# Kernel optimization log

Measured on AMD Instinct MI355X. Metric: run time of the kernel, lower is better.

## Reference

```python
import jax, jax.numpy as jnp
import numpy as np
import math

B, S, D, H = 4, 1024, 1024, 16
HD = D // H
R = 128  # max_rel_pos
EPS = 1e-5

def setup_inputs() -> dict:
    key = jax.random.key(0)
    ks = jax.random.split(key, 20)
    sd = 1.0 / math.sqrt(D)
    def lin(k, din, dout):
        return jax.random.normal(k, (din, dout), jnp.float32) * (1.0 / math.sqrt(din))
    return {
        "x": jax.random.normal(ks[0], (B, S, D), jnp.float32),
        "wq": lin(ks[1], D, D), "bq": jnp.zeros((D,), jnp.float32),
        "wk": lin(ks[2], D, D), "bk": jnp.zeros((D,), jnp.float32),
        "wv": lin(ks[3], D, D), "bv": jnp.zeros((D,), jnp.float32),
        "wo": lin(ks[4], D, D), "bo": jnp.zeros((D,), jnp.float32),
        "rel_embed": jax.random.normal(ks[5], (2 * R + 1, HD), jnp.float32),
        "ln1_g": jnp.ones((D,), jnp.float32), "ln1_b": jnp.zeros((D,), jnp.float32),
        "ln2_g": jnp.ones((D,), jnp.float32), "ln2_b": jnp.zeros((D,), jnp.float32),
        "w1": lin(ks[6], D, 4 * D), "b1": jnp.zeros((4 * D,), jnp.float32),
        "w2": lin(ks[7], 4 * D, D), "b2": jnp.zeros((D,), jnp.float32),
    }

def _layernorm(x, g, b):
    mu = jnp.mean(x, axis=-1, keepdims=True)
    var = jnp.mean(jnp.square(x - mu), axis=-1, keepdims=True)
    return (x - mu) * jax.lax.rsqrt(var + EPS) * g + b

def _block(x, wq, bq, wk, bk, wv, bv, wo, bo, rel_embed,
           ln1_g, ln1_b, ln2_g, ln2_b, w1, b1, w2, b2):
    h = _layernorm(x, ln1_g, ln1_b)
    # project and split heads: [B,S,D] -> [B,H,S,HD]
    def heads(y):
        return y.reshape(B, S, H, HD).transpose(0, 2, 1, 3)
    Q = heads(h @ wq + bq)
    K = heads(h @ wk + bk)
    V = heads(h @ wv + bv)
    scale = 1.0 / math.sqrt(HD)
    scores = jnp.einsum("bhqd,bhkd->bhqk", Q, K) * scale
    # relative positions: clamp(q-k, -R, R) + R
    pos = jnp.arange(S)
    rel_idx = jnp.clip(pos[None, :] - pos[:, None], -R, R) + R  # [S,S]
    rel = rel_embed[rel_idx]  # [S,S,HD]
    scores = scores + jnp.einsum("bhqd,qkd->bhqk", Q, rel) * scale
    attn = jax.nn.softmax(scores, axis=-1)
    out = jnp.einsum("bhqk,bhkd->bhqd", attn, V)
    out = out.transpose(0, 2, 1, 3).reshape(B, S, D) @ wo + bo
    x = x + out  # dropout is identity in eval
    h2 = _layernorm(x, ln2_g, ln2_b)
    ff = jax.nn.gelu(h2 @ w1 + b1, approximate=False) @ w2 + b2
    return x + ff

def reference(x, wq, bq, wk, bk, wv, bv, wo, bo, rel_embed,
              ln1_g, ln1_b, ln2_g, ln2_b, w1, b1, w2, b2):
    return _block(x, wq, bq, wk, bk, wv, bv, wo, bo, rel_embed,
                  ln1_g, ln1_b, ln2_g, ln2_b, w1, b1, w2, b2)
```

## Files before the change

kernel.cpp:

```cpp
#include <hip/hip_runtime.h>

typedef unsigned short u16;
typedef __bf16 bf16x8 __attribute__((ext_vector_type(8)));
typedef float f32x4 __attribute__((ext_vector_type(4)));

#define QSCALE 0.18033688011112042f

__device__ __forceinline__ float b2f(u16 x) {
    unsigned int u = ((unsigned int)x) << 16;
    return __builtin_bit_cast(float, u);
}
__device__ __forceinline__ u16 f2bf(float f) {
    unsigned int u = __builtin_bit_cast(unsigned int, f);
    u += 0x7fffu + ((u >> 16) & 1u);
    return (u16)(u >> 16);
}
__device__ __forceinline__ void lds_load16(const u16* g, u16* l) {
    __builtin_amdgcn_global_load_lds(
        (const __attribute__((address_space(1))) void*)g,
        (__attribute__((address_space(3))) void*)l, 16, 0, 0);
}

__global__ void transpose_f32_bf16(const float* __restrict__ in, u16* __restrict__ out,
                                   int R, int C) {
    __shared__ u16 tile[32][33];
    int bx = blockIdx.x * 32, by = blockIdx.y * 32;
    int tx = threadIdx.x, ty = threadIdx.y;
#pragma unroll
    for (int i = 0; i < 32; i += 8)
        tile[ty + i][tx] = f2bf(in[(size_t)(by + ty + i) * C + bx + tx]);
    __syncthreads();
#pragma unroll
    for (int i = 0; i < 32; i += 8)
        out[(size_t)(bx + ty + i) * R + by + tx] = tile[tx][ty + i];
}

__global__ void transpose_w4(const float* __restrict__ wq, const float* __restrict__ wk,
                             const float* __restrict__ wv, const float* __restrict__ wo,
                             u16* __restrict__ wqkvT, u16* __restrict__ woT) {
    __shared__ u16 tile[32][33];
    int z = blockIdx.z;
    const float* in = (z == 0) ? wq : (z == 1) ? wk : (z == 2) ? wv : wo;
    u16* out = (z < 3) ? (wqkvT + (size_t)z * 1024 * 1024) : woT;
    int bx = blockIdx.x * 32, by = blockIdx.y * 32;
    int tx = threadIdx.x, ty = threadIdx.y;
#pragma unroll
    for (int i = 0; i < 32; i += 8)
        tile[ty + i][tx] = f2bf(in[(size_t)(by + ty + i) * 1024 + bx + tx]);
    __syncthreads();
#pragma unroll
    for (int i = 0; i < 32; i += 8)
        out[(size_t)(bx + ty + i) * 1024 + by + tx] = tile[tx][ty + i];
}

__global__ void transpose_v(const u16* __restrict__ in, int ldin, int coloff,
                            u16* __restrict__ out) {
    __shared__ u16 tile[32][33];
    size_t zout = (size_t)blockIdx.z << 20;
    int bx = blockIdx.x * 32, by = blockIdx.y * 32;
    int tx = threadIdx.x, ty = threadIdx.y;
#pragma unroll
    for (int i = 0; i < 32; i += 8)
        tile[ty + i][tx] =
            in[(size_t)(blockIdx.z * 1024 + by + ty + i) * ldin + coloff + bx + tx];
    __syncthreads();
#pragma unroll
    for (int i = 0; i < 32; i += 8)
        out[zout + (size_t)(bx + ty + i) * 1024 + by + tx] = tile[tx][ty + i];
}

__global__ void cvt_f32_bf16(const float* __restrict__ in, u16* __restrict__ out, int n) {
    int i = blockIdx.x * 256 + threadIdx.x;
    if (i < n) out[i] = f2bf(in[i]);
}

__global__ void concat3(const float* a, const float* b, const float* c, float* o) {
    int i = blockIdx.x * 256 + threadIdx.x;
    o[i] = (i < 1024) ? a[i] : (i < 2048 ? b[i - 1024] : c[i - 2048]);
}

__global__ __launch_bounds__(256) void ln_kernel(
    const u16* __restrict__ inb, const float* __restrict__ inf,
    const float* __restrict__ g, const float* __restrict__ b,
    u16* __restrict__ out) {
    int row = blockIdx.x, t = threadIdx.x;
    size_t base = (size_t)row * 1024 + t * 4;
    float v[4];
    if (inf) {
        float4 f = *(const float4*)(inf + base);
        v[0] = f.x; v[1] = f.y; v[2] = f.z; v[3] = f.w;
    } else {
        uint2 u = *(const uint2*)(inb + base);
        v[0] = b2f((u16)(u.x & 0xffff)); v[1] = b2f((u16)(u.x >> 16));
        v[2] = b2f((u16)(u.y & 0xffff)); v[3] = b2f((u16)(u.y >> 16));
    }
    float s = v[0] + v[1] + v[2] + v[3];
    float q = v[0] * v[0] + v[1] * v[1] + v[2] * v[2] + v[3] * v[3];
#pragma unroll
    for (int m = 1; m < 64; m <<= 1) {
        s += __shfl_xor(s, m);
        q += __shfl_xor(q, m);
    }
    __shared__ float rs[4], rq[4];
    __shared__ float mu_s, rstd_s;
    int w = t >> 6, lane = t & 63;
    if (lane == 0) { rs[w] = s; rq[w] = q; }
    __syncthreads();
    if (t == 0) {
        float S = rs[0] + rs[1] + rs[2] + rs[3];
        float Q2 = rq[0] + rq[1] + rq[2] + rq[3];
        float mu = S * (1.0f / 1024.0f);
        float var = Q2 * (1.0f / 1024.0f) - mu * mu;
        mu_s = mu;
        rstd_s = rsqrtf(var + 1e-5f);
    }
    __syncthreads();
    float mu = mu_s, rstd = rstd_s;
    u16 o[4];
#pragma unroll
    for (int i = 0; i < 4; i++) {
        int col = t * 4 + i;
        o[i] = f2bf((v[i] - mu) * rstd * g[col] + b[col]);
    }
    uint2 pk;
    pk.x = (unsigned)o[0] | ((unsigned)o[1] << 16);
    pk.y = (unsigned)o[2] | ((unsigned)o[3] << 16);
    *(uint2*)(out + base) = pk;
}

__global__ __launch_bounds__(256) void gemm_bt64(
    const u16* __restrict__ A, int lda,
    const u16* __restrict__ Bt, int ldb,
    const float* __restrict__ bias,
    const float* __restrict__ resid_f32, const u16* __restrict__ resid_bf,
    u16* __restrict__ outb, float* __restrict__ outf, int ldc,
    int K, float oscale, int gelu) {
    constexpr int AU = 16, BU = 8, UPW = (AU + BU) / 4;
    __shared__ __align__(16) u16 As[2][128 * 64];
    __shared__ __align__(16) u16 Bs[2][64 * 64];
    int t = threadIdx.x, w = t >> 6, lane = t & 63;
    int m0 = blockIdx.y * 128, n0 = blockIdx.x * 64;
    int lo = lane & 15, hi = lane >> 4;
    int wr = w >> 1, wc = w & 1;
    f32x4 acc[4][2];
#pragma unroll
    for (int i = 0; i < 4; i++)
#pragma unroll
        for (int j = 0; j < 2; j++) acc[i][j] = (f32x4){0.f, 0.f, 0.f, 0.f};

    auto stage = [&](int k0, int buf) {
#pragma unroll
        for (int uu = 0; uu < UPW; ++uu) {
            int u = w * UPW + uu;
            if (u < AU) {
                int s = u * 64 + lane;
                int row = s >> 3, cg = (lane & 7) ^ (row & 7);
                lds_load16(A + (size_t)(m0 + row) * lda + k0 + cg * 8,
                           &As[buf][u * 512]);
            } else {
                int u2 = u - AU;
                int s = u2 * 64 + lane;
                int row = s >> 3, cg = (lane & 7) ^ (row & 7);
                lds_load16(Bt + (size_t)(n0 + row) * ldb + k0 + cg * 8,
                           &Bs[buf][u2 * 512]);
            }
        }
    };

    int nk = K >> 6;
    stage(0, 0);
    for (int kk = 0; kk < nk; ++kk) {
        __syncthreads();
        if (kk + 1 < nk) stage((kk + 1) << 6, (kk + 1) & 1);
        int buf = kk & 1;
#pragma unroll
        for (int k2 = 0; k2 < 2; ++k2) {
            bf16x8 a[4], bb[2];
#pragma unroll
            for (int i = 0; i < 4; i++) {
                int row = wr * 64 + i * 16 + lo;
                int g = (k2 * 4 + hi) ^ (row & 7);
                a[i] = *(const bf16x8*)&As[buf][row * 64 + g * 8];
            }
#pragma unroll
            for (int j = 0; j < 2; j++) {
                int row = wc * 32 + j * 16 + lo;
                int g = (k2 * 4 + hi) ^ (row & 7);
                bb[j] = *(const bf16x8*)&Bs[buf][row * 64 + g * 8];
            }
#pragma unroll
            for (int i = 0; i < 4; i++)
#pragma unroll
                for (int j = 0; j < 2; j++)
                    acc[i][j] = __builtin_amdgcn_mfma_f32_16x16x32_bf16(a[i], bb[j], acc[i][j], 0, 0, 0);
        }
    }
#pragma unroll
    for (int j = 0; j < 2; j++) {
        int col = n0 + wc * 32 + j * 16 + lo;
        float bv = bias ? bias[col] : 0.f;
#pragma unroll
        for (int i = 0; i < 4; i++) {
            int rbase = m0 + wr * 64 + i * 16 + hi * 4;
#pragma unroll
            for (int r = 0; r < 4; r++) {
                float v = fmaf(acc[i][j][r], oscale, bv);
                if (gelu) v = 0.5f * v * (1.f + erff(v * 0.70710678118654752f));
                size_t ridx = (size_t)(rbase + r) * ldc + col;
                if (resid_f32) v += resid_f32[ridx];
                if (resid_bf) v += b2f(resid_bf[ridx]);
                if (outf) outf[ridx] = v;
                if (outb) outb[ridx] = f2bf(v);
            }
        }
    }
}

__global__ __launch_bounds__(256) void gemm_bt128k64(
    const u16* __restrict__ A, int lda,
    const u16* __restrict__ Bt, int ldb,
    const float* __restrict__ bias,
    u16* __restrict__ outb, int ldc,
    int K, float oscale, int gelu) {
    __shared__ __align__(16) u16 As[2][128 * 64];
    __shared__ __align__(16) u16 Bs[2][128 * 64];
    int t = threadIdx.x, w = t >> 6, lane = t & 63;
    int m0 = blockIdx.y * 128, n0 = blockIdx.x * 128;
    int lo = lane & 15, hi = lane >> 4;
    int wr = w >> 1, wc = w & 1;
    f32x4 acc[4][4];
#pragma unroll
    for (int i = 0; i < 4; i++)
#pragma unroll
        for (int j = 0; j < 4; j++) acc[i][j] = (f32x4){0.f, 0.f, 0.f, 0.f};

    auto stage = [&](int k0, int buf) {
#pragma unroll
        for (int uu = 0; uu < 4; ++uu) {
            int u = w * 4 + uu;
            int s = u * 64 + lane;
            int row = s >> 3, cg = (lane & 7) ^ (row & 7);
            lds_load16(A + (size_t)(m0 + row) * lda + k0 + cg * 8,
                       &As[buf][u * 512]);
        }
#pragma unroll
        for (int uu = 0; uu < 4; ++uu) {
            int u = w * 4 + uu;
            int s = u * 64 + lane;
            int row = s >> 3, cg = (lane & 7) ^ (row & 7);
            lds_load16(Bt + (size_t)(n0 + row) * ldb + k0 + cg * 8,
                       &Bs[buf][u * 512]);
        }
    };

    int nk = K >> 6;
    stage(0, 0);
    for (int kk = 0; kk < nk; ++kk) {
        __syncthreads();
        if (kk + 1 < nk) stage((kk + 1) << 6, (kk + 1) & 1);
        int buf = kk & 1;
#pragma unroll
        for (int k2 = 0; k2 < 2; ++k2) {
            bf16x8 a[4], bb[4];
#pragma unroll
            for (int i = 0; i < 4; i++) {
                int row = wr * 64 + i * 16 + lo;
                int g = (k2 * 4 + hi) ^ (row & 7);
                a[i] = *(const bf16x8*)&As[buf][row * 64 + g * 8];
            }
#pragma unroll
            for (int j = 0; j < 4; j++) {
                int row = wc * 64 + j * 16 + lo;
                int g = (k2 * 4 + hi) ^ (row & 7);
                bb[j] = *(const bf16x8*)&Bs[buf][row * 64 + g * 8];
            }
#pragma unroll
            for (int i = 0; i < 4; i++)
#pragma unroll
                for (int j = 0; j < 4; j++)
                    acc[i][j] = __builtin_amdgcn_mfma_f32_16x16x32_bf16(a[i], bb[j], acc[i][j], 0, 0, 0);
        }
    }
#pragma unroll
    for (int j = 0; j < 4; j++) {
        int col = n0 + wc * 64 + j * 16 + lo;
        float bv = bias ? bias[col] : 0.f;
#pragma unroll
        for (int i = 0; i < 4; i++) {
            int rbase = m0 + wr * 64 + i * 16 + hi * 4;
#pragma unroll
            for (int r = 0; r < 4; r++) {
                float v = fmaf(acc[i][j][r], oscale, bv);
                if (gelu) v = 0.5f * v * (1.f + erff(v * 0.70710678118654752f));
                outb[(size_t)(rbase + r) * ldc + col] = f2bf(v);
            }
        }
    }
}

__global__ __launch_bounds__(256) void attn_kernel(
    const u16* __restrict__ QKV, const u16* __restrict__ Vtg,
    const u16* __restrict__ relb, u16* __restrict__ Ob) {
    __shared__ __align__(16) u16 KsL[2][4096];
    __shared__ __align__(16) u16 VsL[2][4096];
    __shared__ __align__(16) u16 Ps[4][16 * 72];
    __shared__ __align__(16) u16 Rb[4][16 * 280];
    int t = threadIdx.x, w = t >> 6, lane = t & 63;
    int bid = blockIdx.x;
    int qblk = bid & 15, h = (bid >> 4) & 15, bb = bid >> 8;
    int lo = lane & 15, hi = lane >> 4;
    int q0b = qblk * 64;
    int q0 = q0b + w * 16;

    const u16* qrow = QKV + ((size_t)(bb * 1024 + q0 + lo) * 3072 + h * 64 + hi * 8);
    bf16x8 qf0 = *(const bf16x8*)qrow;
    bf16x8 qf1 = *(const bf16x8*)(qrow + 32);

    const u16* Kg = QKV + 1024 + ((size_t)(bb * 1024)) * 3072 + h * 64;
    const u16* Vg = Vtg + ((size_t)(bb * 1024 + h * 64)) * 1024;

    auto stage = [&](int k0, int buf) {
#pragma unroll
        for (int half = 0; half < 2; ++half) {
            int s = half * 256 + w * 64 + lane;
            int row = s >> 3, cg = (s & 7) ^ (row & 7);
            lds_load16(Kg + (size_t)(k0 + row) * 3072 + cg * 8,
                       &KsL[buf][(half * 256 + w * 64) * 8]);
            lds_load16(Vg + (size_t)row * 1024 + k0 + cg * 8,
                       &VsL[buf][(half * 256 + w * 64) * 8]);
        }
    };

    stage(0, 0);

#pragma unroll 4
    for (int pt = 0; pt < 17; ++pt) {
        bf16x8 rf0 = *(const bf16x8*)&relb[(pt * 16 + lo) * 64 + hi * 8];
        bf16x8 rf1 = *(const bf16x8*)&relb[(pt * 16 + lo) * 64 + 32 + hi * 8];
        f32x4 cz = (f32x4){0.f, 0.f, 0.f, 0.f};
        cz = __builtin_amdgcn_mfma_f32_16x16x32_bf16(qf0, rf0, cz, 0, 0, 0);
        cz = __builtin_amdgcn_mfma_f32_16x16x32_bf16(qf1, rf1, cz, 0, 0, 0);
#pragma unroll
        for (int r = 0; r < 4; r++)
            Rb[w][(hi * 4 + r) * 280 + pt * 16 + lo] =
                f2bf(fmaf(cz[r], QSCALE, -16.0f));
    }
    float blo[4], bhi[4];
#pragma unroll
    for (int r = 0; r < 4; r++) {
        blo[r] = b2f(Rb[w][(hi * 4 + r) * 280]);
        bhi[r] = b2f(Rb[w][(hi * 4 + r) * 280 + 256]);
    }

    f32x4 oacc[4];
#pragma unroll
    for (int j = 0; j < 4; j++) oacc[j] = (f32x4){0.f, 0.f, 0.f, 0.f};
    float l_[4] = {0.f, 0.f, 0.f, 0.f};

    for (int c = 0; c < 16; ++c) {
        int k0 = c * 64;
        __syncthreads();
        if (c < 15) stage(k0 + 64, (c + 1) & 1);
        const u16* Ksb = KsL[c & 1];
        const u16* Vsb = VsL[c & 1];

        f32x4 sc[4];
#pragma unroll
        for (int kt = 0; kt < 4; kt++) {
            int row = kt * 16 + lo, rx = row & 7;
            bf16x8 kf0 = *(const bf16x8*)&Ksb[(row * 8 + (hi ^ rx)) * 8];
            bf16x8 kf1 = *(const bf16x8*)&Ksb[(row * 8 + ((4 + hi) ^ rx)) * 8];
            f32x4 zz = (f32x4){0.f, 0.f, 0.f, 0.f};
            sc[kt] = __builtin_amdgcn_mfma_f32_16x16x32_bf16(qf0, kf0, zz, 0, 0, 0);
            sc[kt] = __builtin_amdgcn_mfma_f32_16x16x32_bf16(qf1, kf1, sc[kt], 0, 0, 0);
        }
        float bt[4][4];
        if (k0 + 192 <= q0b) {
#pragma unroll
            for (int kt = 0; kt < 4; kt++)
#pragma unroll
                for (int r = 0; r < 4; r++) bt[kt][r] = blo[r];
        } else if (k0 >= q0b + 192) {
#pragma unroll
            for (int kt = 0; kt < 4; kt++)
#pragma unroll
                for (int r = 0; r < 4; r++) bt[kt][r] = bhi[r];
        } else {
#pragma unroll
            for (int kt = 0; kt < 4; kt++)
#pragma unroll
                for (int r = 0; r < 4; r++) {
                    int lq = hi * 4 + r;
                    int p = (k0 + kt * 16 + lo) - (q0 + lq);
                    p = p < -128 ? -128 : (p > 128 ? 128 : p);
                    p += 128;
                    bt[kt][r] = b2f(Rb[w][lq * 280 + p]);
                }
        }
#pragma unroll
        for (int kt = 0; kt < 4; kt++)
#pragma unroll
            for (int r = 0; r < 4; r++) {
                float s = fmaf(sc[kt][r], QSCALE, bt[kt][r]);
                float p = __builtin_amdgcn_exp2f(s);
                l_[r] += p;
                Ps[w][(hi * 4 + r) * 72 + kt * 16 + lo] =
                    (u16)(__builtin_bit_cast(unsigned int, p) >> 16);
            }
        bf16x8 pf0 = *(const bf16x8*)&Ps[w][lo * 72 + 8 * hi];
        bf16x8 pf1 = *(const bf16x8*)&Ps[w][lo * 72 + 32 + 8 * hi];
#pragma unroll
        for (int j = 0; j < 4; j++) {
            int row = j * 16 + lo, rx = row & 7;
            bf16x8 vf0 = *(const bf16x8*)&Vsb[(row * 8 + (hi ^ rx)) * 8];
            bf16x8 vf1 = *(const bf16x8*)&Vsb[(row * 8 + ((4 + hi) ^ rx)) * 8];
            oacc[j] = __builtin_amdgcn_mfma_f32_16x16x32_bf16(pf0, vf0, oacc[j], 0, 0, 0);
            oacc[j] = __builtin_amdgcn_mfma_f32_16x16x32_bf16(pf1, vf1, oacc[j], 0, 0, 0);
        }
    }
#pragma unroll
    for (int r = 0; r < 4; r++) {
#pragma unroll
        for (int m = 1; m < 16; m <<= 1) l_[r] += __shfl_xor(l_[r], m);
    }
#pragma unroll
    for (int r = 0; r < 4; r++) {
        float inv = 1.f / l_[r];
        int q = q0 + hi * 4 + r;
#pragma unroll
        for (int j = 0; j < 4; j++)
            Ob[(size_t)(bb * 1024 + q) * 1024 + h * 64 + j * 16 + lo] =
                f2bf(oacc[j][r] * inv);
    }
}

extern "C" void kernel_launch(void* const* d_in, const int* in_sizes, int n_in,
                              void* d_out, int out_size, void* d_ws, size_t ws_size,
                              hipStream_t stream) {
    const float* x   = (const float*)d_in[0];
    const float* wq  = (const float*)d_in[1];
    const float* bq  = (const float*)d_in[2];
    const float* wk  = (const float*)d_in[3];
    const float* bk  = (const float*)d_in[4];
    const float* wv  = (const float*)d_in[5];
    const float* bv  = (const float*)d_in[6];
    const float* wo  = (const float*)d_in[7];
    const float* bo  = (const float*)d_in[8];
    const float* rel = (const float*)d_in[9];
    const float* g1  = (const float*)d_in[10];
    const float* be1 = (const float*)d_in[11];
    const float* g2  = (const float*)d_in[12];
    const float* be2 = (const float*)d_in[13];
    const float* w1  = (const float*)d_in[14];
    const float* bf1 = (const float*)d_in[15];
    const float* w2  = (const float*)d_in[16];
    const float* bf2 = (const float*)d_in[17];

    char* ws = (char*)d_ws;
    const size_t MB = 1024ull * 1024ull;
    u16* wqkvT = (u16*)(ws + 0 * MB);
    u16* woT  = (u16*)(ws + 6 * MB);
    u16* w1T  = (u16*)(ws + 8 * MB);
    u16* w2T  = (u16*)(ws + 16 * MB);
    u16* h    = (u16*)(ws + 24 * MB);
    u16* QKV  = (u16*)(ws + 32 * MB);
    u16* Vtg  = (u16*)(ws + 56 * MB);
    u16* x2b  = (u16*)(ws + 64 * MB);
    u16* att  = (u16*)(ws + 112 * MB);
    u16* relb = (u16*)(ws + 120 * MB);
    float* bqkv = (float*)(ws + 120 * MB + 128 * 1024);
    u16* ff1  = (u16*)(ws + 32 * MB);
    u16* h2   = h;

    dim3 tb(32, 8);
    transpose_w4<<<dim3(32, 32, 4), tb, 0, stream>>>(wq, wk, wv, wo, wqkvT, woT);
    transpose_f32_bf16<<<dim3(128, 32), tb, 0, stream>>>(w1, w1T, 1024, 4096);
    transpose_f32_bf16<<<dim3(32, 128), tb, 0, stream>>>(w2, w2T, 4096, 1024);
    cvt_f32_bf16<<<65, 256, 0, stream>>>(rel, relb, 257 * 64);
    concat3<<<12, 256, 0, stream>>>(bq, bk, bv, bqkv);

    ln_kernel<<<4096, 256, 0, stream>>>(nullptr, x, g1, be1, h);

    gemm_bt128k64<<<dim3(24, 32), 256, 0, stream>>>(h, 1024, wqkvT, 1024,
        bqkv, QKV, 3072, 1024, 1.f, 0);
    transpose_v<<<dim3(32, 32, 4), tb, 0, stream>>>(QKV, 3072, 2048, Vtg);

    attn_kernel<<<1024, 256, 0, stream>>>(QKV, Vtg, relb, att);

    gemm_bt64<<<dim3(16, 32), 256, 0, stream>>>(att, 1024, woT, 1024,
        bo, x, nullptr, x2b, nullptr, 1024, 1024, 1.f, 0);

    ln_kernel<<<4096, 256, 0, stream>>>(x2b, nullptr, g2, be2, h2);

    gemm_bt128k64<<<dim3(32, 32), 256, 0, stream>>>(h2, 1024, w1T, 1024,
        bf1, ff1, 4096, 1024, 1.f, 1);
    gemm_bt64<<<dim3(16, 32), 256, 0, stream>>>(ff1, 4096, w2T, 4096,
        bf2, nullptr, x2b, nullptr, (float*)d_out, 1024, 4096, 1.f, 0);
}
```

Measured before the change: 394.5 us.

## Merge weight prep kernels into one launch and use 128-tile GEMM for FFN2

Folds the four weight transposes, the rel-embed conversion and the bias concat into a single prep_kernel launch, which cuts kernel launch overhead. Extends gemm_bt128k64 with an optional bf16 residual input and an fp32 output. The FFN down-projection now runs on this 128x128 K64 GEMM instead of gemm_bt64. That launches 256 blocks instead of 512, so each block does more reuse per K step at the cost of lower occupancy across CUs.

```diff
diff --git a/kernel.cpp b/kernel.cpp
--- a/kernel.cpp
+++ b/kernel.cpp
@@ -21,36 +21,53 @@
         (__attribute__((address_space(3))) void*)l, 16, 0, 0);
 }
 
-__global__ void transpose_f32_bf16(const float* __restrict__ in, u16* __restrict__ out,
-                                   int R, int C) {
-    __shared__ u16 tile[32][33];
-    int bx = blockIdx.x * 32, by = blockIdx.y * 32;
+__global__ void prep_kernel(
+    const float* __restrict__ wq, const float* __restrict__ wk,
+    const float* __restrict__ wv, const float* __restrict__ wo,
+    const float* __restrict__ w1, const float* __restrict__ w2,
+    const float* __restrict__ rel,
+    const float* __restrict__ bq, const float* __restrict__ bk,
+    const float* __restrict__ bv,
+    u16* __restrict__ wqkvT, u16* __restrict__ woT,
+    u16* __restrict__ w1T, u16* __restrict__ w2T,
+    u16* __restrict__ relb, float* __restrict__ bqkv) {
+    int bid = blockIdx.x;
     int tx = threadIdx.x, ty = threadIdx.y;
-#pragma unroll
-    for (int i = 0; i < 32; i += 8)
-        tile[ty + i][tx] = f2bf(in[(size_t)(by + ty + i) * C + bx + tx]);
-    __syncthreads();
-#pragma unroll
-    for (int i = 0; i < 32; i += 8)
-        out[(size_t)(bx + ty + i) * R + by + tx] = tile[tx][ty + i];
-}
-
-__global__ void transpose_w4(const float* __restrict__ wq, const float* __restrict__ wk,
-                             const float* __restrict__ wv, const float* __restrict__ wo,
-                             u16* __restrict__ wqkvT, u16* __restrict__ woT) {
-    __shared__ u16 tile[32][33];
-    int z = blockIdx.z;
-    const float* in = (z == 0) ? wq : (z == 1) ? wk : (z == 2) ? wv : wo;
-    u16* out = (z < 3) ? (wqkvT + (size_t)z * 1024 * 1024) : woT;
-    int bx = blockIdx.x * 32, by = blockIdx.y * 32;
-    int tx = threadIdx.x, ty = threadIdx.y;
-#pragma unroll
-    for (int i = 0; i < 32; i += 8)
-        tile[ty + i][tx] = f2bf(in[(size_t)(by + ty + i) * 1024 + bx + tx]);
-    __syncthreads();
-#pragma unroll
-    for (int i = 0; i < 32; i += 8)
-        out[(size_t)(bx + ty + i) * 1024 + by + tx] = tile[tx][ty + i];
+    if (bid < 12288) {
+        __shared__ u16 tile[32][33];
+        const float* in;
+        u16* out;
+        int R, C, bx, by;
+        if (bid < 4096) {
+            int z = bid >> 10, i = bid & 1023;
+            in = (z == 0) ? wq : (z == 1) ? wk : (z == 2) ? wv : wo;
+            out = (z < 3) ? wqkvT + (size_t)z * 1024 * 1024 : woT;
+            R = 1024; C = 1024;
+            bx = (i & 31) * 32; by = (i >> 5) * 32;
+        } else if (bid < 8192) {
+            int i = bid - 4096;
+            in = w1; out = w1T; R = 1024; C = 4096;
+            bx = (i & 127) * 32; by = (i >> 7) * 32;
+        } else {
+            int i = bid - 8192;
+            in = w2; out = w2T; R = 4096; C = 1024;
+            bx = (i & 31) * 32; by = (i >> 5) * 32;
+        }
+#pragma unroll
+        for (int i = 0; i < 32; i += 8)
+            tile[ty + i][tx] = f2bf(in[(size_t)(by + ty + i) * C + bx + tx]);
+        __syncthreads();
+#pragma unroll
+        for (int i = 0; i < 32; i += 8)
+            out[(size_t)(bx + ty + i) * R + by + tx] = tile[tx][ty + i];
+    } else if (bid < 12353) {
+        int i = (bid - 12288) * 256 + ty * 32 + tx;
+        if (i < 257 * 64) relb[i] = f2bf(rel[i]);
+    } else {
+        int i = (bid - 12353) * 256 + ty * 32 + tx;
+        if (i < 3072)
+            bqkv[i] = (i < 1024) ? bq[i] : (i < 2048 ? bk[i - 1024] : bv[i - 2048]);
+    }
 }
 
 __global__ void transpose_v(const u16* __restrict__ in, int ldin, int coloff,
@@ -67,16 +84,6 @@
 #pragma unroll
     for (int i = 0; i < 32; i += 8)
         out[zout + (size_t)(bx + ty + i) * 1024 + by + tx] = tile[tx][ty + i];
-}
-
-__global__ void cvt_f32_bf16(const float* __restrict__ in, u16* __restrict__ out, int n) {
-    int i = blockIdx.x * 256 + threadIdx.x;
-    if (i < n) out[i] = f2bf(in[i]);
-}
-
-__global__ void concat3(const float* a, const float* b, const float* c, float* o) {
-    int i = blockIdx.x * 256 + threadIdx.x;
-    o[i] = (i < 1024) ? a[i] : (i < 2048 ? b[i - 1024] : c[i - 2048]);
 }
 
 __global__ __launch_bounds__(256) void ln_kernel(
@@ -219,8 +226,8 @@
 __global__ __launch_bounds__(256) void gemm_bt128k64(
     const u16* __restrict__ A, int lda,
     const u16* __restrict__ Bt, int ldb,
-    const float* __restrict__ bias,
-    u16* __restrict__ outb, int ldc,
+    const float* __restrict__ bias, const u16* __restrict__ resid_bf,
+    u16* __restrict__ outb, float* __restrict__ outf, int ldc,
     int K, float oscale, int gelu) {
     __shared__ __align__(16) u16 As[2][128 * 64];
     __shared__ __align__(16) u16 Bs[2][128 * 64];
@@ -292,7 +299,10 @@
             for (int r = 0; r < 4; r++) {
                 float v = fmaf(acc[i][j][r], oscale, bv);
                 if (gelu) v = 0.5f * v * (1.f + erff(v * 0.70710678118654752f));
-                outb[(size_t)(rbase + r) * ldc + col] = f2bf(v);
+                size_t ridx = (size_t)(rbase + r) * ldc + col;
+                if (resid_bf) v += b2f(resid_bf[ridx]);
+                if (outf) outf[ridx] = v;
+                if (outb) outb[ridx] = f2bf(v);
             }
         }
     }
@@ -473,16 +483,14 @@
     u16* h2   = h;
 
     dim3 tb(32, 8);
-    transpose_w4<<<dim3(32, 32, 4), tb, 0, stream>>>(wq, wk, wv, wo, wqkvT, woT);
-    transpose_f32_bf16<<<dim3(128, 32), tb, 0, stream>>>(w1, w1T, 1024, 4096);
-    transpose_f32_bf16<<<dim3(32, 128), tb, 0, stream>>>(w2, w2T, 4096, 1024);
-    cvt_f32_bf16<<<65, 256, 0, stream>>>(rel, relb, 257 * 64);
-    concat3<<<12, 256, 0, stream>>>(bq, bk, bv, bqkv);
+    prep_kernel<<<12365, tb, 0, stream>>>(wq, wk, wv, wo, w1, w2, rel,
+                                          bq, bk, bv,
+                                          wqkvT, woT, w1T, w2T, relb, bqkv);
 
     ln_kernel<<<4096, 256, 0, stream>>>(nullptr, x, g1, be1, h);
 
     gemm_bt128k64<<<dim3(24, 32), 256, 0, stream>>>(h, 1024, wqkvT, 1024,
-        bqkv, QKV, 3072, 1024, 1.f, 0);
+        bqkv, nullptr, QKV, nullptr, 3072, 1024, 1.f, 0);
     transpose_v<<<dim3(32, 32, 4), tb, 0, stream>>>(QKV, 3072, 2048, Vtg);
 
     attn_kernel<<<1024, 256, 0, stream>>>(QKV, Vtg, relb, att);
@@ -493,7 +501,7 @@
     ln_kernel<<<4096, 256, 0, stream>>>(x2b, nullptr, g2, be2, h2);
 
     gemm_bt128k64<<<dim3(32, 32), 256, 0, stream>>>(h2, 1024, w1T, 1024,
-        bf1, ff1, 4096, 1024, 1.f, 1);
-    gemm_bt64<<<dim3(16, 32), 256, 0, stream>>>(ff1, 4096, w2T, 4096,
-        bf2, nullptr, x2b, nullptr, (float*)d_out, 1024, 4096, 1.f, 0);
-}
+        bf1, nullptr, ff1, nullptr, 4096, 1024, 1.f, 1);
+    gemm_bt128k64<<<dim3(8, 32), 256, 0, stream>>>(ff1, 4096, w2T, 4096,
+        bf2, x2b, nullptr, (float*)d_out, 1024, 4096, 1.f, 0);
+}
```

Result: slower. 415.0 us (+5.2%).
